# Kernel tuning notes

Hardware: AMD Instinct MI355X
Metric: run time of the kernel (lower is better)

The kernel has to match this reference:

```python
import jax, jax.numpy as jnp
import numpy as np

GAMMA = 0.99
LMBDA = 0.95


def setup_inputs() -> dict:
    key = jax.random.key(0)
    k1, k2, k3, k4 = jax.random.split(key, 4)
    B, T = 4096, 2048
    return {
        "reward": jax.random.normal(k1, (B, T), dtype=jnp.float32),
        "terminated": jax.random.randint(k2, (B, T), 0, 2, dtype=jnp.int32),
        "value": jax.random.normal(k3, (B, T), dtype=jnp.float32),
        "next_value": jax.random.normal(k4, (B, T), dtype=jnp.float32),
    }


def _gae(reward, not_done, value, next_value):
    # All inputs [B, T]. Backward-time scan over T with carry gae [B].
    # delta_t = r_t + gamma * V(s_{t+1}) * nd_t - V(s_t)
    # A_t = delta_t + gamma * lmbda * nd_t * A_{t+1}
    xs = (reward.T, not_done.T, value.T, next_value.T)  # each [T, B]

    def step(gae, x):
        r, nd, v, nv = x
        delta = r + GAMMA * nv * nd - v
        gae = delta + GAMMA * LMBDA * nd * gae
        return gae, gae

    init = jnp.zeros(reward.shape[0], dtype=reward.dtype)
    _, adv_t = jax.lax.scan(step, init, xs, reverse=True)  # [T, B]
    advantages = adv_t.T  # [B, T]
    returns = advantages + value
    return advantages, returns


def reference(reward, terminated, value, next_value):
    not_done = 1.0 - terminated.astype(reward.dtype)
    return _gae(reward, not_done, value, next_value)
```

## Files before the change

### kernel.cpp

```cpp
#include <hip/hip_runtime.h>


constexpr float GAMMA = 0.99f;
constexpr float LMBDA = 0.95f;
constexpr int   T     = 2048;
constexpr int   TPB   = 512;
constexpr int   E     = T / TPB;
constexpr int   NW    = TPB / 64;

typedef float f4 __attribute__((ext_vector_type(4)));

__global__ __launch_bounds__(TPB) void gae_kernel(
    const float* __restrict__ reward,
    const int*   __restrict__ term,
    const float* __restrict__ value,
    const float* __restrict__ next_value,
    float* __restrict__ adv_out,
    float* __restrict__ ret_out)
{
    const int j    = threadIdx.x;
    const int wave = j >> 6;
    const int lane = j & 63;
    const size_t base = (size_t)blockIdx.x * T + (size_t)j * E;

    const float4 rv = ((const float4*)(reward     + base))[0];
    const int4   tv = ((const int4*  )(term       + base))[0];
    const float4 vv = ((const float4*)(value      + base))[0];
    const float4 nv = ((const float4*)(next_value + base))[0];

    const float r [E] = {rv.x, rv.y, rv.z, rv.w};
    const float nd[E] = {1.f - (float)tv.x, 1.f - (float)tv.y,
                         1.f - (float)tv.z, 1.f - (float)tv.w};
    const float v [E] = {vv.x, vv.y, vv.z, vv.w};
    const float nx[E] = {nv.x, nv.y, nv.z, nv.w};

    float loc[E], P[E];
    {
        float g = 0.f, p = 1.f;
        #pragma unroll
        for (int t = E - 1; t >= 0; --t) {
            const float c     = (GAMMA * LMBDA) * nd[t];
            const float delta = fmaf(GAMMA * nx[t], nd[t], r[t]) - v[t];
            g = fmaf(c, g, delta);
            p *= c;
            loc[t] = g;
            P[t]   = p;
        }
    }

    float A = loc[0], Bc = P[0];
    #pragma unroll
    for (int off = 1; off < 64; off <<= 1) {
        const float a2 = __shfl_down(A,  off, 64);
        const float b2 = __shfl_down(Bc, off, 64);
        if (lane + off < 64) {
            A  = fmaf(Bc, a2, A);
            Bc *= b2;
        }
    }

    __shared__ float sA[NW], sB[NW];
    if (lane == 0) { sA[wave] = A; sB[wave] = Bc; }

    float eA = __shfl_down(A,  1, 64);
    float eB = __shfl_down(Bc, 1, 64);
    if (lane == 63) { eA = 0.f; eB = 1.f; }

    __syncthreads();

    float wcarry = 0.f;
    #pragma unroll
    for (int w = NW - 1; w > 0; --w) {
        if (w > wave) wcarry = fmaf(sB[w], wcarry, sA[w]);
    }

    const float gin = fmaf(eB, wcarry, eA);

    f4 a4, q4;
    #pragma unroll
    for (int t = 0; t < E; ++t) {
        const float a = fmaf(P[t], gin, loc[t]);
        a4[t] = a;
        q4[t] = a + v[t];
    }
    __builtin_nontemporal_store(a4, (f4*)(adv_out + base));
    __builtin_nontemporal_store(q4, (f4*)(ret_out + base));
}

extern "C" void kernel_launch(void* const* d_in, const int* in_sizes, int n_in,
                              void* d_out, int out_size, void* d_ws, size_t ws_size,
                              hipStream_t stream) {
    const float* reward     = (const float*)d_in[0];
    const int*   term       = (const int*  )d_in[1];
    const float* value      = (const float*)d_in[2];
    const float* next_value = (const float*)d_in[3];

    const int BT = in_sizes[0];
    const int B  = BT / T;

    float* adv = (float*)d_out;
    float* ret = adv + BT;

    gae_kernel<<<B, TPB, 0, stream>>>(reward, term, value, next_value, adv, ret);
}
```

Baseline: 174.5 us.

## Stage rows into LDS with async global_load_lds and process four rows per block

Each block now handles four rows in sequence, loading inputs directly into shared memory via global_load_lds and prefetching the next row while the current row is scanned. Wave carries use double-buffered shared arrays so only one barrier is needed per row. The aim is to overlap global loads with compute and cut launch and block overhead. In exchange the block uses 32KB of LDS and manual waitcnt handling. The ordering of the vmcnt waits across waves is subtle and may race, since other waves' async LDS writes are not covered by a barrier.

```diff
diff --git a/kernel.cpp b/kernel.cpp
--- a/kernel.cpp
+++ b/kernel.cpp
@@ -1,4 +1,5 @@
 #include <hip/hip_runtime.h>
+#include <stdint.h>
 
 
 constexpr float GAMMA = 0.99f;
@@ -7,10 +8,18 @@
 constexpr int   TPB   = 512;
 constexpr int   E     = T / TPB;
 constexpr int   NW    = TPB / 64;
+constexpr int   RPB   = 4;
 
 typedef float f4 __attribute__((ext_vector_type(4)));
 
-__global__ __launch_bounds__(TPB) void gae_kernel(
+typedef __attribute__((address_space(1))) void  as1_void;
+typedef __attribute__((address_space(3))) void  as3_void;
+
+__device__ __forceinline__ void stage16(const void* g, void* s) {
+    __builtin_amdgcn_global_load_lds((as1_void*)g, (as3_void*)s, 16, 0, 0);
+}
+
+__global__ __launch_bounds__(TPB, 8) void gae_kernel(
     const float* __restrict__ reward,
     const int*   __restrict__ term,
     const float* __restrict__ value,
@@ -21,70 +30,103 @@
     const int j    = threadIdx.x;
     const int wave = j >> 6;
     const int lane = j & 63;
-    const size_t base = (size_t)blockIdx.x * T + (size_t)j * E;
 
-    const float4 rv = ((const float4*)(reward     + base))[0];
-    const int4   tv = ((const int4*  )(term       + base))[0];
-    const float4 vv = ((const float4*)(value      + base))[0];
-    const float4 nv = ((const float4*)(next_value + base))[0];
+    __shared__ float sRew[T];
+    __shared__ int   sTrm[T];
+    __shared__ float sVal[T];
+    __shared__ float sNxt[T];
+    __shared__ float sAf[2][NW];
+    __shared__ float sBf[2][NW];
 
-    const float r [E] = {rv.x, rv.y, rv.z, rv.w};
-    const float nd[E] = {1.f - (float)tv.x, 1.f - (float)tv.y,
-                         1.f - (float)tv.z, 1.f - (float)tv.w};
-    const float v [E] = {vv.x, vv.y, vv.z, vv.w};
-    const float nx[E] = {nv.x, nv.y, nv.z, nv.w};
+    const size_t tbase = (size_t)blockIdx.x * (RPB * T) + (size_t)j * E;
+    const int    wofs  = wave << 8;
 
-    float loc[E], P[E];
-    {
-        float g = 0.f, p = 1.f;
+    stage16(reward     + tbase, sRew + wofs);
+    stage16(term       + tbase, sTrm + wofs);
+    stage16(value      + tbase, sVal + wofs);
+    stage16(next_value + tbase, sNxt + wofs);
+    asm volatile("s_waitcnt vmcnt(0)" ::: "memory");
+
+    #pragma unroll 1
+    for (int k = 0; k < RPB; ++k) {
+        asm volatile("s_waitcnt vmcnt(2)" ::: "memory");
+
+        const f4   rv = *(const f4*  )(sRew + j * E);
+        const int4 tv = *(const int4*)(sTrm + j * E);
+        const f4   vv = *(const f4*  )(sVal + j * E);
+        const f4   nx = *(const f4*  )(sNxt + j * E);
+
+        asm volatile("s_waitcnt lgkmcnt(0)" ::: "memory");
+        if (k + 1 < RPB) {
+            const size_t nb = tbase + (size_t)(k + 1) * T;
+            stage16(reward     + nb, sRew + wofs);
+            stage16(term       + nb, sTrm + wofs);
+            stage16(value      + nb, sVal + wofs);
+            stage16(next_value + nb, sNxt + wofs);
+        }
+        asm volatile("" ::: "memory");
+
+        const float r [E] = {rv[0], rv[1], rv[2], rv[3]};
+        const float nd[E] = {1.f - (float)tv.x, 1.f - (float)tv.y,
+                             1.f - (float)tv.z, 1.f - (float)tv.w};
+        const float v [E] = {vv[0], vv[1], vv[2], vv[3]};
+        const float nxv[E]= {nx[0], nx[1], nx[2], nx[3]};
+
+        float loc[E], P[E];
+        {
+            float g = 0.f, p = 1.f;
+            #pragma unroll
+            for (int t = E - 1; t >= 0; --t) {
+                const float c     = (GAMMA * LMBDA) * nd[t];
+                const float delta = fmaf(GAMMA * nxv[t], nd[t], r[t]) - v[t];
+                g = fmaf(c, g, delta);
+                p *= c;
+                loc[t] = g;
+                P[t]   = p;
+            }
+        }
+
+        float A = loc[0], Bc = P[0];
         #pragma unroll
-        for (int t = E - 1; t >= 0; --t) {
-            const float c     = (GAMMA * LMBDA) * nd[t];
-            const float delta = fmaf(GAMMA * nx[t], nd[t], r[t]) - v[t];
-            g = fmaf(c, g, delta);
-            p *= c;
-            loc[t] = g;
-            P[t]   = p;
+        for (int off = 1; off < 64; off <<= 1) {
+            const float a2 = __shfl_down(A,  off, 64);
+            const float b2 = __shfl_down(Bc, off, 64);
+            if (lane + off < 64) {
+                A  = fmaf(Bc, a2, A);
+                Bc *= b2;
+            }
         }
+
+        const int pb = k & 1;
+        if (lane == 0) { sAf[pb][wave] = A; sBf[pb][wave] = Bc; }
+
+        float eA = __shfl_down(A,  1, 64);
+        float eB = __shfl_down(Bc, 1, 64);
+        if (lane == 63) { eA = 0.f; eB = 1.f; }
+
+        asm volatile("s_waitcnt lgkmcnt(0)" ::: "memory");
+        __builtin_amdgcn_s_barrier();
+        asm volatile("" ::: "memory");
+
+        float wcarry = 0.f;
+        #pragma unroll
+        for (int w = NW - 1; w > 0; --w) {
+            if (w > wave) wcarry = fmaf(sBf[pb][w], wcarry, sAf[pb][w]);
+        }
+
+        const float gin = fmaf(eB, wcarry, eA);
+
+        f4 a4, q4;
+        #pragma unroll
+        for (int t = 0; t < E; ++t) {
+            const float a = fmaf(P[t], gin, loc[t]);
+            a4[t] = a;
+            q4[t] = a + v[t];
+        }
+        const size_t gb = tbase + (size_t)k * T;
+        __builtin_nontemporal_store(a4, (f4*)(adv_out + gb));
+        __builtin_nontemporal_store(q4, (f4*)(ret_out + gb));
     }
-
-    float A = loc[0], Bc = P[0];
-    #pragma unroll
-    for (int off = 1; off < 64; off <<= 1) {
-        const float a2 = __shfl_down(A,  off, 64);
-        const float b2 = __shfl_down(Bc, off, 64);
-        if (lane + off < 64) {
-            A  = fmaf(Bc, a2, A);
-            Bc *= b2;
-        }
-    }
-
-    __shared__ float sA[NW], sB[NW];
-    if (lane == 0) { sA[wave] = A; sB[wave] = Bc; }
-
-    float eA = __shfl_down(A,  1, 64);
-    float eB = __shfl_down(Bc, 1, 64);
-    if (lane == 63) { eA = 0.f; eB = 1.f; }
-
-    __syncthreads();
-
-    float wcarry = 0.f;
-    #pragma unroll
-    for (int w = NW - 1; w > 0; --w) {
-        if (w > wave) wcarry = fmaf(sB[w], wcarry, sA[w]);
-    }
-
-    const float gin = fmaf(eB, wcarry, eA);
-
-    f4 a4, q4;
-    #pragma unroll
-    for (int t = 0; t < E; ++t) {
-        const float a = fmaf(P[t], gin, loc[t]);
-        a4[t] = a;
-        q4[t] = a + v[t];
-    }
-    __builtin_nontemporal_store(a4, (f4*)(adv_out + base));
-    __builtin_nontemporal_store(q4, (f4*)(ret_out + base));
 }
 
 extern "C" void kernel_launch(void* const* d_in, const int* in_sizes, int n_in,
@@ -101,5 +143,5 @@
     float* adv = (float*)d_out;
     float* ret = adv + BT;
 
-    gae_kernel<<<B, TPB, 0, stream>>>(reward, term, value, next_value, adv, ret);
+    gae_kernel<<<B / RPB, TPB, 0, stream>>>(reward, term, value, next_value, adv, ret);
 }
```

Measured after the change: 178.3 us. 2.2% more time.

## Process four rows per block with 8 elements per thread and prefetch next row

Applied to the files above, without the earlier changes.

Each block now handles four rows with 256 threads and 8 elements per thread, and loads the next row's inputs while scanning the current one. Double-buffered shared slots allow a single raw barrier per row. The aim is to hide global memory latency behind the scan and to cut block launch and sync overhead in this memory-bound kernel. In exchange it raises register pressure and launches fewer blocks, so fewer waves are in flight.

```diff
diff --git a/kernel.cpp b/kernel.cpp
--- a/kernel.cpp
+++ b/kernel.cpp
@@ -3,14 +3,37 @@
 
 constexpr float GAMMA = 0.99f;
 constexpr float LMBDA = 0.95f;
+constexpr float GL    = GAMMA * LMBDA;
 constexpr int   T     = 2048;
-constexpr int   TPB   = 512;
+constexpr int   TPB   = 256;
 constexpr int   E     = T / TPB;
 constexpr int   NW    = TPB / 64;
+constexpr int   RPB   = 4;
 
 typedef float f4 __attribute__((ext_vector_type(4)));
 
-__global__ __launch_bounds__(TPB) void gae_kernel(
+struct RowRegs {
+    f4   r0, r1;
+    int4 t0, t1;
+    f4   v0, v1;
+    f4   n0, n1;
+};
+
+__device__ __forceinline__ RowRegs load_row(const float* __restrict__ rew,
+                                            const int*   __restrict__ trm,
+                                            const float* __restrict__ val,
+                                            const float* __restrict__ nxt,
+                                            size_t base)
+{
+    RowRegs R;
+    R.r0 = *(const f4*  )(rew + base);  R.r1 = *(const f4*  )(rew + base + 4);
+    R.t0 = *(const int4*)(trm + base);  R.t1 = *(const int4*)(trm + base + 4);
+    R.v0 = *(const f4*  )(val + base);  R.v1 = *(const f4*  )(val + base + 4);
+    R.n0 = *(const f4*  )(nxt + base);  R.n1 = *(const f4*  )(nxt + base + 4);
+    return R;
+}
+
+__global__ __launch_bounds__(TPB, 4) void gae_kernel(
     const float* __restrict__ reward,
     const int*   __restrict__ term,
     const float* __restrict__ value,
@@ -21,70 +44,92 @@
     const int j    = threadIdx.x;
     const int wave = j >> 6;
     const int lane = j & 63;
-    const size_t base = (size_t)blockIdx.x * T + (size_t)j * E;
 
-    const float4 rv = ((const float4*)(reward     + base))[0];
-    const int4   tv = ((const int4*  )(term       + base))[0];
-    const float4 vv = ((const float4*)(value      + base))[0];
-    const float4 nv = ((const float4*)(next_value + base))[0];
+    __shared__ float sAf[2][NW];
+    __shared__ float sBf[2][NW];
 
-    const float r [E] = {rv.x, rv.y, rv.z, rv.w};
-    const float nd[E] = {1.f - (float)tv.x, 1.f - (float)tv.y,
-                         1.f - (float)tv.z, 1.f - (float)tv.w};
-    const float v [E] = {vv.x, vv.y, vv.z, vv.w};
-    const float nx[E] = {nv.x, nv.y, nv.z, nv.w};
+    const size_t tbase = (size_t)blockIdx.x * (RPB * T) + (size_t)j * E;
 
-    float loc[E], P[E];
-    {
-        float g = 0.f, p = 1.f;
+    RowRegs cur = load_row(reward, term, value, next_value, tbase);
+
+    #pragma unroll
+    for (int k = 0; k < RPB; ++k) {
+        RowRegs nxt;
+        if (k + 1 < RPB)
+            nxt = load_row(reward, term, value, next_value,
+                           tbase + (size_t)(k + 1) * T);
+
+        const float r [E] = {cur.r0[0], cur.r0[1], cur.r0[2], cur.r0[3],
+                             cur.r1[0], cur.r1[1], cur.r1[2], cur.r1[3]};
+        const float nd[E] = {1.f - (float)cur.t0.x, 1.f - (float)cur.t0.y,
+                             1.f - (float)cur.t0.z, 1.f - (float)cur.t0.w,
+                             1.f - (float)cur.t1.x, 1.f - (float)cur.t1.y,
+                             1.f - (float)cur.t1.z, 1.f - (float)cur.t1.w};
+        const float v [E] = {cur.v0[0], cur.v0[1], cur.v0[2], cur.v0[3],
+                             cur.v1[0], cur.v1[1], cur.v1[2], cur.v1[3]};
+        const float nx[E] = {cur.n0[0], cur.n0[1], cur.n0[2], cur.n0[3],
+                             cur.n1[0], cur.n1[1], cur.n1[2], cur.n1[3]};
+
+        float loc[E], P[E];
+        {
+            float g = 0.f, p = 1.f;
+            #pragma unroll
+            for (int t = E - 1; t >= 0; --t) {
+                const float c     = GL * nd[t];
+                const float delta = fmaf(GAMMA * nx[t], nd[t], r[t]) - v[t];
+                g = fmaf(c, g, delta);
+                p *= c;
+                loc[t] = g;
+                P[t]   = p;
+            }
+        }
+
+        float A = loc[0], Bc = P[0];
         #pragma unroll
-        for (int t = E - 1; t >= 0; --t) {
-            const float c     = (GAMMA * LMBDA) * nd[t];
-            const float delta = fmaf(GAMMA * nx[t], nd[t], r[t]) - v[t];
-            g = fmaf(c, g, delta);
-            p *= c;
-            loc[t] = g;
-            P[t]   = p;
+        for (int off = 1; off < 64; off <<= 1) {
+            const float a2 = __shfl_down(A,  off, 64);
+            const float b2 = __shfl_down(Bc, off, 64);
+            if (lane + off < 64) {
+                A  = fmaf(Bc, a2, A);
+                Bc *= b2;
+            }
         }
+
+        const int pb = k & 1;
+        if (lane == 0) { sAf[pb][wave] = A; sBf[pb][wave] = Bc; }
+
+        float eA = __shfl_down(A,  1, 64);
+        float eB = __shfl_down(Bc, 1, 64);
+        if (lane == 63) { eA = 0.f; eB = 1.f; }
+
+        asm volatile("s_waitcnt lgkmcnt(0)" ::: "memory");
+        __builtin_amdgcn_s_barrier();
+        asm volatile("" ::: "memory");
+
+        float wcarry = 0.f;
+        #pragma unroll
+        for (int w = NW - 1; w > 0; --w) {
+            if (w > wave) wcarry = fmaf(sBf[pb][w], wcarry, sAf[pb][w]);
+        }
+
+        const float gin = fmaf(eB, wcarry, eA);
+
+        f4 a0, a1, q0, q1;
+        #pragma unroll
+        for (int t = 0; t < 4; ++t) {
+            const float aa = fmaf(P[t], gin, loc[t]);
+            const float ab = fmaf(P[t + 4], gin, loc[t + 4]);
+            a0[t] = aa;  q0[t] = aa + v[t];
+            a1[t] = ab;  q1[t] = ab + v[t + 4];
+        }
+        const size_t gb = tbase + (size_t)k * T;
+        __builtin_nontemporal_store(a0, (f4*)(adv_out + gb));
+        __builtin_nontemporal_store(a1, (f4*)(adv_out + gb + 4));
+        __builtin_nontemporal_store(q0, (f4*)(ret_out + gb));
+        __builtin_nontemporal_store(q1, (f4*)(ret_out + gb + 4));
+
+        if (k + 1 < RPB) cur = nxt;
     }
-
-    float A = loc[0], Bc = P[0];
-    #pragma unroll
-    for (int off = 1; off < 64; off <<= 1) {
-        const float a2 = __shfl_down(A,  off, 64);
-        const float b2 = __shfl_down(Bc, off, 64);
-        if (lane + off < 64) {
-            A  = fmaf(Bc, a2, A);
-            Bc *= b2;
-        }
-    }
-
-    __shared__ float sA[NW], sB[NW];
-    if (lane == 0) { sA[wave] = A; sB[wave] = Bc; }
-
-    float eA = __shfl_down(A,  1, 64);
-    float eB = __shfl_down(Bc, 1, 64);
-    if (lane == 63) { eA = 0.f; eB = 1.f; }
-
-    __syncthreads();
-
-    float wcarry = 0.f;
-    #pragma unroll
-    for (int w = NW - 1; w > 0; --w) {
-        if (w > wave) wcarry = fmaf(sB[w], wcarry, sA[w]);
-    }
-
-    const float gin = fmaf(eB, wcarry, eA);
-
-    f4 a4, q4;
-    #pragma unroll
-    for (int t = 0; t < E; ++t) {
-        const float a = fmaf(P[t], gin, loc[t]);
-        a4[t] = a;
-        q4[t] = a + v[t];
-    }
-    __builtin_nontemporal_store(a4, (f4*)(adv_out + base));
-    __builtin_nontemporal_store(q4, (f4*)(ret_out + base));
 }
 
 extern "C" void kernel_launch(void* const* d_in, const int* in_sizes, int n_in,
@@ -101,5 +146,5 @@
     float* adv = (float*)d_out;
     float* ret = adv + BT;
 
-    gae_kernel<<<B, TPB, 0, stream>>>(reward, term, value, next_value, adv, ret);
+    gae_kernel<<<B / RPB, TPB, 0, stream>>>(reward, term, value, next_value, adv, ret);
 }
```

Measured after the change: 184.7 us. 1.06x slower.

## Assign one wave per row with 32 elements per lane, removing block sync

Applied to the files above, without the earlier changes.

Each wavefront now processes a whole row, with each lane owning 32 contiguous timesteps loaded as eight float4 chunks. The cross-wave shared-memory carry and __syncthreads are removed, and a second serial pass over the lane's elements replaces the stored prefix products. The aim is to drop block-level synchronisation and increase per-thread work, at the cost of strided per-instruction memory access, higher register use and a longer serial dependency chain.

```diff
diff --git a/kernel.cpp b/kernel.cpp
--- a/kernel.cpp
+++ b/kernel.cpp
@@ -3,10 +3,12 @@
 
 constexpr float GAMMA = 0.99f;
 constexpr float LMBDA = 0.95f;
+constexpr float GL    = GAMMA * LMBDA;
 constexpr int   T     = 2048;
-constexpr int   TPB   = 512;
-constexpr int   E     = T / TPB;
-constexpr int   NW    = TPB / 64;
+constexpr int   TPB   = 256;
+constexpr int   WPB   = TPB / 64;
+constexpr int   EPL   = T / 64;
+constexpr int   NF4   = EPL / 4;
 
 typedef float f4 __attribute__((ext_vector_type(4)));
 
@@ -18,37 +20,41 @@
     float* __restrict__ adv_out,
     float* __restrict__ ret_out)
 {
-    const int j    = threadIdx.x;
-    const int wave = j >> 6;
-    const int lane = j & 63;
-    const size_t base = (size_t)blockIdx.x * T + (size_t)j * E;
+    const int lane = threadIdx.x & 63;
+    const int wave = threadIdx.x >> 6;
+    const int row  = blockIdx.x * WPB + wave;
+    const size_t base = (size_t)row * T + (size_t)lane * EPL;
 
-    const float4 rv = ((const float4*)(reward     + base))[0];
-    const int4   tv = ((const int4*  )(term       + base))[0];
-    const float4 vv = ((const float4*)(value      + base))[0];
-    const float4 nv = ((const float4*)(next_value + base))[0];
+    float c[EPL], d[EPL], v[EPL];
+    #pragma unroll
+    for (int q = 0; q < NF4; ++q) {
+        const size_t o = base + 4 * q;
+        const f4   rv = *(const f4*  )(reward     + o);
+        const int4 tv = *(const int4*)(term       + o);
+        const f4   vv = *(const f4*  )(value      + o);
+        const f4   nx = *(const f4*  )(next_value + o);
+        const int ti[4] = {tv.x, tv.y, tv.z, tv.w};
+        #pragma unroll
+        for (int u = 0; u < 4; ++u) {
+            const int   t  = 4 * q + u;
+            const float nd = 1.f - (float)ti[u];
+            v[t] = vv[u];
+            c[t] = GL * nd;
+            d[t] = fmaf(GAMMA * nx[u], nd, rv[u]) - vv[u];
+        }
+    }
 
-    const float r [E] = {rv.x, rv.y, rv.z, rv.w};
-    const float nd[E] = {1.f - (float)tv.x, 1.f - (float)tv.y,
-                         1.f - (float)tv.z, 1.f - (float)tv.w};
-    const float v [E] = {vv.x, vv.y, vv.z, vv.w};
-    const float nx[E] = {nv.x, nv.y, nv.z, nv.w};
-
-    float loc[E], P[E];
+    float A, Bc;
     {
         float g = 0.f, p = 1.f;
         #pragma unroll
-        for (int t = E - 1; t >= 0; --t) {
-            const float c     = (GAMMA * LMBDA) * nd[t];
-            const float delta = fmaf(GAMMA * nx[t], nd[t], r[t]) - v[t];
-            g = fmaf(c, g, delta);
-            p *= c;
-            loc[t] = g;
-            P[t]   = p;
+        for (int t = EPL - 1; t >= 0; --t) {
+            g = fmaf(c[t], g, d[t]);
+            p *= c[t];
         }
+        A = g; Bc = p;
     }
 
-    float A = loc[0], Bc = P[0];
     #pragma unroll
     for (int off = 1; off < 64; off <<= 1) {
         const float a2 = __shfl_down(A,  off, 64);
@@ -59,32 +65,31 @@
         }
     }
 
-    __shared__ float sA[NW], sB[NW];
-    if (lane == 0) { sA[wave] = A; sB[wave] = Bc; }
+    float gin = __shfl_down(A, 1, 64);
+    if (lane == 63) gin = 0.f;
 
-    float eA = __shfl_down(A,  1, 64);
-    float eB = __shfl_down(Bc, 1, 64);
-    if (lane == 63) { eA = 0.f; eB = 1.f; }
-
-    __syncthreads();
-
-    float wcarry = 0.f;
-    #pragma unroll
-    for (int w = NW - 1; w > 0; --w) {
-        if (w > wave) wcarry = fmaf(sB[w], wcarry, sA[w]);
+    {
+        float g = gin;
+        #pragma unroll
+        for (int t = EPL - 1; t >= 0; --t) {
+            g = fmaf(c[t], g, d[t]);
+            d[t] = g;
+        }
     }
 
-    const float gin = fmaf(eB, wcarry, eA);
-
-    f4 a4, q4;
     #pragma unroll
-    for (int t = 0; t < E; ++t) {
-        const float a = fmaf(P[t], gin, loc[t]);
-        a4[t] = a;
-        q4[t] = a + v[t];
+    for (int q = 0; q < NF4; ++q) {
+        const size_t o = base + 4 * q;
+        f4 a4, q4;
+        #pragma unroll
+        for (int u = 0; u < 4; ++u) {
+            const int t = 4 * q + u;
+            a4[u] = d[t];
+            q4[u] = d[t] + v[t];
+        }
+        __builtin_nontemporal_store(a4, (f4*)(adv_out + o));
+        __builtin_nontemporal_store(q4, (f4*)(ret_out + o));
     }
-    __builtin_nontemporal_store(a4, (f4*)(adv_out + base));
-    __builtin_nontemporal_store(q4, (f4*)(ret_out + base));
 }
 
 extern "C" void kernel_launch(void* const* d_in, const int* in_sizes, int n_in,
@@ -101,5 +106,5 @@
     float* adv = (float*)d_out;
     float* ret = adv + BT;
 
-    gae_kernel<<<B, TPB, 0, stream>>>(reward, term, value, next_value, adv, ret);
+    gae_kernel<<<B / WPB, TPB, 0, stream>>>(reward, term, value, next_value, adv, ret);
 }
```

Measured after the change: 308.4 us. 1.77x slower.
